# Kernel tuning notes

Hardware: AMD Instinct MI355X
Metric: run time of the kernel (lower is better)

Reference implementation:

```python
import jax, jax.numpy as jnp
import numpy as np

EPS = 1e-5
K_GROUP = 8  # k_group_size


def setup_inputs() -> dict:
    key = jax.random.key(0)
    ks = jax.random.split(key, 8)
    C = 384  # encoder_channel
    rn = lambda k, s: (jax.random.normal(k, s, dtype=jnp.float32) * 0.05)
    return {
        "point_groups": jax.random.normal(ks[0], (4, 256, 32, 3), dtype=jnp.float32),
        # first_conv: Conv1d(3,128,1)+BN+ReLU+Conv1d(128,256,1)
        "W1": rn(ks[1], (128, 3)), "b1": jnp.zeros(128, jnp.float32),
        "gamma1": jnp.ones(128, jnp.float32), "beta1": jnp.zeros(128, jnp.float32),
        "W2": rn(ks[2], (256, 128)), "b2": jnp.zeros(256, jnp.float32),
        # second_conv: Conv1d(512,512,1)+BN+ReLU+Conv1d(512,C,1)
        "W3": rn(ks[3], (512, 512)), "b3": jnp.zeros(512, jnp.float32),
        "gamma3": jnp.ones(512, jnp.float32), "beta3": jnp.zeros(512, jnp.float32),
        "W4": rn(ks[4], (C, 512)), "b4": jnp.zeros(C, jnp.float32),
        # K_Norm affine (out_dim = C, matching declared parameter shapes)
        "alpha": jnp.ones((1, 1, 1, C), jnp.float32),
        "beta_aff": jnp.zeros((1, 1, 1, C), jnp.float32),
        # fusion_layer: Conv1d(2C,C,1)+BN+ReLU
        "Wf": rn(ks[5], (C, 2 * C)), "bf": jnp.zeros(C, jnp.float32),
        "gammaf": jnp.ones(C, jnp.float32), "betaf": jnp.zeros(C, jnp.float32),
    }


def _conv1x1(x, W, b):  # x: (B,Cin,L), W: (Cout,Cin)
    return jnp.einsum("bcl,oc->bol", x, W) + b[None, :, None]


def _bn(x, gamma, beta):  # training-mode BatchNorm1d over (batch, length)
    mu = jnp.mean(x, axis=(0, 2), keepdims=True)
    var = jnp.var(x, axis=(0, 2), keepdims=True)
    xh = (x - mu) * jax.lax.rsqrt(var + EPS)
    return xh * gamma[None, :, None] + beta[None, :, None]


def reference(point_groups, W1, b1, gamma1, beta1, W2, b2, W3, b3, gamma3, beta3,
              W4, b4, alpha, beta_aff, Wf, bf, gammaf, betaf):
    bs, g, n, _ = point_groups.shape
    C = W4.shape[0]
    pg = point_groups.reshape(bs * g, n, 3)  # (B', n, 3)

    # first_conv stack
    f = _conv1x1(pg.transpose(0, 2, 1), W1, b1)           # (B',128,n)
    f = jax.nn.relu(_bn(f, gamma1, beta1))
    f = _conv1x1(f, W2, b2)                               # (B',256,n)
    fg = jnp.max(f, axis=2, keepdims=True)                # (B',256,1)
    f = jnp.concatenate([jnp.broadcast_to(fg, f.shape), f], axis=1)  # (B',512,n)

    # second_conv stack
    f = _conv1x1(f, W3, b3)
    f = jax.nn.relu(_bn(f, gamma3, beta3))
    f = _conv1x1(f, W4, b4)                               # (B',C,n)
    feat = f.transpose(0, 2, 1)                           # (B',n,C)

    # KNN within each group (self included, as in KNN(xyz,xyz))
    sq = jnp.sum(pg * pg, axis=-1)                        # (B',n)
    d = sq[:, :, None] + sq[:, None, :] - 2.0 * jnp.einsum("bnc,bmc->bnm", pg, pg)
    _, idx = jax.lax.top_k(-d, K_GROUP)                   # (B',n,K)

    gather = jax.vmap(lambda a, i: a[i])
    knn_x = gather(feat, idx)                             # (B',n,K,C)

    # K_Norm: center-relative normalization by global scalar std (torch.std, ddof=1)
    mean_x = feat[:, :, None, :]
    dx = knn_x - mean_x
    std_x = jnp.std(dx, ddof=1)
    knn_x = dx / (std_x + EPS)
    knn_x = alpha * knn_x + beta_aff                      # (B',n,K,C)

    enhanced = jnp.mean(knn_x, axis=2)                    # mean over K -> (B',n,C)
    enhanced = jnp.mean(enhanced, axis=1)                 # pool over n -> (B',C)

    fg2 = jnp.max(f, axis=2)                              # (B',C)
    fused_in = jnp.concatenate([fg2, enhanced], axis=1)[:, :, None]  # (B',2C,1)
    fused = jax.nn.relu(_bn(_conv1x1(fused_in, Wf, bf), gammaf, betaf))[:, :, 0]
    return fused.reshape(bs, g, C)
```

## Files before the change

kernel.cpp:

```cpp
#include <hip/hip_runtime.h>
#include <math.h>

#define EPS 1e-5f

typedef __attribute__((ext_vector_type(8))) short s16x8;
typedef __attribute__((ext_vector_type(4))) float f32x4;

__device__ __forceinline__ unsigned short f2bf(float x) {
    unsigned u = __float_as_uint(x);
    u += 0x7fffu + ((u >> 16) & 1u);
    return (unsigned short)(u >> 16);
}
__device__ __forceinline__ float bf2f(unsigned short h) {
    return __uint_as_float(((unsigned)h) << 16);
}
__device__ __forceinline__ unsigned long long pack4bf(float a, float b, float c, float d) {
    return (unsigned long long)f2bf(a)
         | ((unsigned long long)f2bf(b) << 16)
         | ((unsigned long long)f2bf(c) << 32)
         | ((unsigned long long)f2bf(d) << 48);
}

template<int CTRL>
__device__ __forceinline__ float dppmov(float x) {
    return __int_as_float(__builtin_amdgcn_update_dpp(
        0, __float_as_int(x), CTRL, 0xF, 0xF, true));
}
__device__ __forceinline__ float red16_sum(float x) {
    x += dppmov<0xB1>(x);
    x += dppmov<0x4E>(x);
    x += dppmov<0x141>(x);
    x += dppmov<0x140>(x);
    return x;
}
__device__ __forceinline__ float red16_max(float x) {
    x = fmaxf(x, dppmov<0xB1>(x));
    x = fmaxf(x, dppmov<0x4E>(x));
    x = fmaxf(x, dppmov<0x141>(x));
    x = fmaxf(x, dppmov<0x140>(x));
    return x;
}

__global__ __launch_bounds__(128) void k1_conv1_knn(
    const float* __restrict__ pg, const float* __restrict__ W1,
    const float* __restrict__ b1,
    const float* __restrict__ W2, const float* __restrict__ W3,
    const float* __restrict__ W4, const float* __restrict__ Wf,
    unsigned short* __restrict__ h1b, float* __restrict__ p1s, float* __restrict__ p1q,
    int* __restrict__ idxw,
    unsigned short* __restrict__ W2b, unsigned short* __restrict__ W3b,
    unsigned short* __restrict__ W4b, unsigned short* __restrict__ Wfb)
{
    __shared__ float pgs[96];
    __shared__ float sqs[32];
    if (blockIdx.x >= 1024) {
        const int i = (blockIdx.x - 1024) * 128 + threadIdx.x;
        if (i < 32768)  W2b[i] = f2bf(W2[i]);
        if (i < 262144) W3b[i] = f2bf(W3[i]);
        if (i < 196608) W4b[i] = f2bf(W4[i]);
        if (i < 294912) Wfb[i] = f2bf(Wf[i]);
        return;
    }
    const int b = blockIdx.x;
    const int t = threadIdx.x;
    if (t < 96) pgs[t] = pg[b * 96 + t];
    __syncthreads();
    if (t < 32) {
        float x = pgs[t*3+0], y = pgs[t*3+1], z = pgs[t*3+2];
        sqs[t] = x*x + y*y + z*z;
    }
    __syncthreads();
    {
        const float w0 = W1[t*3+0], w1 = W1[t*3+1], w2 = W1[t*3+2];
        const float bb = b1[t];
        float s = 0.f, q = 0.f;
        unsigned short* hcol = h1b + (size_t)b*4096 + t;
        #pragma unroll
        for (int l = 0; l < 32; ++l) {
            float v = fmaf(w2, pgs[l*3+2], fmaf(w1, pgs[l*3+1], fmaf(w0, pgs[l*3+0], bb)));
            hcol[l*128] = f2bf(v); s += v; q += v*v;
        }
        p1s[b*128 + t] = s;
        p1q[b*128 + t] = q;
    }
    if (t < 32) {
        const float xl = pgs[t*3+0], yl = pgs[t*3+1], zl = pgs[t*3+2];
        const float sql = sqs[t];
        float dist[32];
        #pragma unroll
        for (int m = 0; m < 32; ++m) {
            float dot = xl*pgs[m*3+0] + yl*pgs[m*3+1] + zl*pgs[m*3+2];
            dist[m] = sql + sqs[m] - 2.f*dot;
        }
        unsigned used = 0u;
        int* orow = idxw + b*256 + t*8;
        #pragma unroll
        for (int j = 0; j < 8; ++j) {
            float best = 3.4e38f; int bi = 0;
            #pragma unroll
            for (int m = 0; m < 32; ++m) {
                if (!((used >> m) & 1u) && dist[m] < best) { best = dist[m]; bi = m; }
            }
            used |= (1u << bi);
            orow[j] = bi;
        }
    }
}

__global__ __launch_bounds__(256) void k_bn_fin2(
    const float* __restrict__ ps, const float* __restrict__ pq,
    int nPart, int nChan, float invN,
    const float* __restrict__ gamma, const float* __restrict__ beta,
    float* __restrict__ scale, float* __restrict__ shift)
{
    const int ob = blockIdx.x * 4;
    const int t = threadIdx.x;
    const int co = t & 3, i0 = t >> 2;
    float s = 0.f, q = 0.f;
    for (int i = i0; i < nPart; i += 64) {
        s += ps[(size_t)i*nChan + ob + co];
        q += pq[(size_t)i*nChan + ob + co];
    }
    #pragma unroll
    for (int off = 32; off >= 4; off >>= 1) {
        s += __shfl_down(s, off, 64);
        q += __shfl_down(q, off, 64);
    }
    __shared__ float ss[4][4], qs[4][4];
    const int wid = t >> 6, lane = t & 63;
    if (lane < 4) { ss[wid][lane] = s; qs[wid][lane] = q; }
    __syncthreads();
    if (t < 4) {
        float S = ss[0][t] + ss[1][t] + ss[2][t] + ss[3][t];
        float Q = qs[0][t] + qs[1][t] + qs[2][t] + qs[3][t];
        const int o = ob + t;
        float mu  = S * invN;
        float var = Q * invN - mu*mu;
        float sc  = gamma[o] * rsqrtf(var + EPS);
        scale[o] = sc;
        shift[o] = beta[o] - mu * sc;
    }
}

__global__ __launch_bounds__(1024, 8) void k3_mfma(
    const unsigned short* __restrict__ h1b,
    const float* __restrict__ scale1, const float* __restrict__ shift1,
    const unsigned short* __restrict__ W2b, const float* __restrict__ b2,
    const unsigned short* __restrict__ W3b, const float* __restrict__ b3,
    unsigned short* __restrict__ h3b, float* __restrict__ p3s, float* __restrict__ p3q)
{
    const int g0 = blockIdx.x * 2;
    const int t = threadIdx.x;
    __shared__ __align__(16) unsigned short SB[26128];
    unsigned short* B1  = SB;
    unsigned short* F2  = SB + 8704;
    unsigned short* FGB = SB + 25600;

    {
        const int l = t >> 4, c0 = (t & 15) * 8;
        const int g = g0 + (l >> 5);
        s16x8 hv = *(const s16x8*)(h1b + (size_t)g*4096 + (l & 31)*128 + c0);
        unsigned short ov[8];
        #pragma unroll
        for (int e = 0; e < 8; ++e) {
            int c = c0 + e;
            float v = fmaxf(fmaf(bf2f((unsigned short)hv[e]), scale1[c], shift1[c]), 0.f);
            ov[e] = f2bf(v);
        }
        uint4 o4;
        o4.x = (unsigned)ov[0] | ((unsigned)ov[1] << 16);
        o4.y = (unsigned)ov[2] | ((unsigned)ov[3] << 16);
        o4.z = (unsigned)ov[4] | ((unsigned)ov[5] << 16);
        o4.w = (unsigned)ov[6] | ((unsigned)ov[7] << 16);
        *(uint4*)&B1[l*136 + c0] = o4;
    }
    __syncthreads();

    const int wave = t >> 6;
    const int lane = t & 63;
    const int m    = lane & 15;
    const int quad = lane >> 4;

    f32x4 acc2[4];
    #pragma unroll
    for (int n = 0; n < 4; ++n)
        acc2[n] = (f32x4){0.f, 0.f, 0.f, 0.f};

    #pragma unroll
    for (int kt = 0; kt < 4; ++kt) {
        s16x8 bv[4];
        #pragma unroll
        for (int nt = 0; nt < 4; ++nt)
            bv[nt] = *(const s16x8*)&B1[(nt*16 + m)*136 + kt*32 + quad*8];
        s16x8 av = *(const s16x8*)(W2b + (size_t)(wave*16 + m)*128 + kt*32 + quad*8);
        #pragma unroll
        for (int nt = 0; nt < 4; ++nt)
            acc2[nt] = __builtin_amdgcn_mfma_f32_16x16x32_bf16(av, bv[nt], acc2[nt], 0, 0, 0);
    }

    {
        const int o0 = wave*16 + quad*4;
        #pragma unroll
        for (int r = 0; r < 4; ++r) {
            float bb = b2[o0 + r];
            #pragma unroll
            for (int nt = 0; nt < 4; ++nt) acc2[nt][r] += bb;
        }
        #pragma unroll
        for (int nt = 0; nt < 4; ++nt) {
            const int row = nt*16 + m;
            *(unsigned long long*)&F2[row*264 + o0] =
                pack4bf(acc2[nt][0], acc2[nt][1], acc2[nt][2], acc2[nt][3]);
        }
        float f0[4], f1[4];
        #pragma unroll
        for (int r = 0; r < 4; ++r) {
            f0[r] = red16_max(fmaxf(acc2[0][r], acc2[1][r]));
            f1[r] = red16_max(fmaxf(acc2[2][r], acc2[3][r]));
        }
        if (m == 0) {
            *(unsigned long long*)&FGB[o0]       = pack4bf(f0[0], f0[1], f0[2], f0[3]);
            *(unsigned long long*)&FGB[264 + o0] = pack4bf(f1[0], f1[1], f1[2], f1[3]);
        }
    }
    __syncthreads();

    unsigned short* dst = h3b + (size_t)blockIdx.x * 32768;
    #pragma unroll
    for (int mt = 0; mt < 2; ++mt) {
        const int ot = wave*2 + mt;
        const int o0 = ot*16 + quad*4;

        f32x4 facc = (f32x4){0.f, 0.f, 0.f, 0.f};
        #pragma unroll
        for (int kt = 0; kt < 8; ++kt) {
            s16x8 bg = *(const s16x8*)&FGB[(m & 1)*264 + kt*32 + quad*8];
            s16x8 av = *(const s16x8*)(W3b + (size_t)(ot*16 + m)*512 + kt*32 + quad*8);
            facc = __builtin_amdgcn_mfma_f32_16x16x32_bf16(av, bg, facc, 0, 0, 0);
        }

        f32x4 acc3[4];
        #pragma unroll
        for (int r = 0; r < 4; ++r) {
            float self = facc[r];
            float oth  = dppmov<0xB1>(self);
            float fg_g0 = (m & 1) ? oth : self;
            float fg_g1 = (m & 1) ? self : oth;
            float bb = b3[o0 + r];
            acc3[0][r] = bb + fg_g0;
            acc3[1][r] = bb + fg_g0;
            acc3[2][r] = bb + fg_g1;
            acc3[3][r] = bb + fg_g1;
        }

        #pragma unroll
        for (int kt = 0; kt < 8; ++kt) {
            s16x8 bv[4];
            #pragma unroll
            for (int nt = 0; nt < 4; ++nt)
                bv[nt] = *(const s16x8*)&F2[(nt*16 + m)*264 + kt*32 + quad*8];
            s16x8 av = *(const s16x8*)(W3b + (size_t)(ot*16 + m)*512 + 256 + kt*32 + quad*8);
            #pragma unroll
            for (int nt = 0; nt < 4; ++nt)
                acc3[nt] = __builtin_amdgcn_mfma_f32_16x16x32_bf16(av, bv[nt], acc3[nt], 0, 0, 0);
        }

        float s[4], q[4];
        #pragma unroll
        for (int r = 0; r < 4; ++r) {
            float x0 = acc3[0][r], x1 = acc3[1][r];
            float x2 = acc3[2][r], x3 = acc3[3][r];
            s[r] = (x0 + x1) + (x2 + x3);
            q[r] = (x0*x0 + x1*x1) + (x2*x2 + x3*x3);
        }
        {
            unsigned long long u0 = pack4bf(acc3[0][0], acc3[0][1], acc3[0][2], acc3[0][3]);
            unsigned long long u1 = pack4bf(acc3[1][0], acc3[1][1], acc3[1][2], acc3[1][3]);
            unsigned long long u2 = pack4bf(acc3[2][0], acc3[2][1], acc3[2][2], acc3[2][3]);
            unsigned long long u3 = pack4bf(acc3[3][0], acc3[3][1], acc3[3][2], acc3[3][3]);
            unsigned short* p = dst + (size_t)(ot*64 + lane) * 16;
            *(uint4*)(p)     = make_uint4((unsigned)u0, (unsigned)(u0 >> 32), (unsigned)u1, (unsigned)(u1 >> 32));
            *(uint4*)(p + 8) = make_uint4((unsigned)u2, (unsigned)(u2 >> 32), (unsigned)u3, (unsigned)(u3 >> 32));
        }
        #pragma unroll
        for (int r = 0; r < 4; ++r) {
            s[r] = red16_sum(s[r]);
            q[r] = red16_sum(q[r]);
        }
        if (m == 0) {
            #pragma unroll
            for (int r = 0; r < 4; ++r) {
                p3s[(size_t)blockIdx.x*512 + o0 + r] = s[r];
                p3q[(size_t)blockIdx.x*512 + o0 + r] = q[r];
            }
        }
    }
}

__global__ __launch_bounds__(512, 4) void k5_mfma(
    const unsigned short* __restrict__ h3b,
    const float* __restrict__ scale3, const float* __restrict__ shift3,
    const unsigned short* __restrict__ W4b, const float* __restrict__ b4,
    const int* __restrict__ idxw,
    float* __restrict__ fg2, float* __restrict__ A,
    float* __restrict__ S1p, float* __restrict__ S2p)
{
    const int g0 = blockIdx.x * 2;
    const int t = threadIdx.x;
    __shared__ __align__(16) unsigned short SB[33280];
    unsigned short* B4 = SB;
    unsigned short* XT = SB;
    unsigned short* Mm = SB + 30720;
    __shared__ int icnt[2][32];
    __shared__ float r1[2][8], r2[2][8];

    {
        const uint4* src = (const uint4*)(h3b + (size_t)blockIdx.x * 32768);
        for (int i = t; i < 4096; i += 512) {
            uint4 hv = src[i];
            const int flat16 = i >> 1, half = i & 1;
            const int ln = flat16 & 63, m2 = ln & 15, q2 = ln >> 4;
            const int wm = flat16 >> 6;
            const int o0 = wm*16 + q2*4;
            const float4 sc = *(const float4*)(scale3 + o0);
            const float4 sh = *(const float4*)(shift3 + o0);
            const int rowa = (half*2)*16 + m2;
            float a0 = fmaxf(fmaf(bf2f((unsigned short)(hv.x       )), sc.x, sh.x), 0.f);
            float a1 = fmaxf(fmaf(bf2f((unsigned short)(hv.x >> 16 )), sc.y, sh.y), 0.f);
            float a2 = fmaxf(fmaf(bf2f((unsigned short)(hv.y       )), sc.z, sh.z), 0.f);
            float a3 = fmaxf(fmaf(bf2f((unsigned short)(hv.y >> 16 )), sc.w, sh.w), 0.f);
            float b0 = fmaxf(fmaf(bf2f((unsigned short)(hv.z       )), sc.x, sh.x), 0.f);
            float b1 = fmaxf(fmaf(bf2f((unsigned short)(hv.z >> 16 )), sc.y, sh.y), 0.f);
            float b2 = fmaxf(fmaf(bf2f((unsigned short)(hv.w       )), sc.z, sh.z), 0.f);
            float b3 = fmaxf(fmaf(bf2f((unsigned short)(hv.w >> 16 )), sc.w, sh.w), 0.f);
            *(unsigned long long*)&B4[rowa*520 + o0]        = pack4bf(a0, a1, a2, a3);
            *(unsigned long long*)&B4[(rowa + 16)*520 + o0] = pack4bf(b0, b1, b2, b3);
        }
    }
    if (t < 64) icnt[t >> 5][t & 31] = 0;
    __syncthreads();

    const int wave = t >> 6;
    const int lane = t & 63;
    const int m    = lane & 15;
    const int quad = lane >> 4;

    f32x4 acc4[3][4];
    #pragma unroll
    for (int mt = 0; mt < 3; ++mt)
        #pragma unroll
        for (int n = 0; n < 4; ++n)
            acc4[mt][n] = (f32x4){0.f, 0.f, 0.f, 0.f};

    #pragma unroll 4
    for (int kt = 0; kt < 16; ++kt) {
        s16x8 bv[4];
        #pragma unroll
        for (int nt = 0; nt < 4; ++nt)
            bv[nt] = *(const s16x8*)&B4[(nt*16 + m)*520 + kt*32 + quad*8];
        #pragma unroll
        for (int mt = 0; mt < 3; ++mt) {
            s16x8 av = *(const s16x8*)(W4b + (size_t)(wave*48 + mt*16 + m)*512 + kt*32 + quad*8);
            #pragma unroll
            for (int nt = 0; nt < 4; ++nt)
                acc4[mt][nt] = __builtin_amdgcn_mfma_f32_16x16x32_bf16(av, bv[nt], acc4[mt][nt], 0, 0, 0);
        }
    }

    #pragma unroll
    for (int mt = 0; mt < 3; ++mt) {
        const int o0 = wave*48 + mt*16 + quad*4;
        float f0[4], f1[4];
        #pragma unroll
        for (int r = 0; r < 4; ++r) {
            float bb = b4[o0 + r];
            #pragma unroll
            for (int nt = 0; nt < 4; ++nt) acc4[mt][nt][r] += bb;
            f0[r] = red16_max(fmaxf(acc4[mt][0][r], acc4[mt][1][r]));
            f1[r] = red16_max(fmaxf(acc4[mt][2][r], acc4[mt][3][r]));
        }
        if (m == 0) {
            #pragma unroll
            for (int r = 0; r < 4; ++r) {
                fg2[(size_t)g0*384 + o0 + r]     = f0[r];
                fg2[(size_t)(g0+1)*384 + o0 + r] = f1[r];
            }
        }
    }
    __syncthreads();

    #pragma unroll
    for (int mt = 0; mt < 3; ++mt) {
        const int o0 = wave*48 + mt*16 + quad*4;
        #pragma unroll
        for (int nt = 0; nt < 4; ++nt) {
            const int g = nt >> 1;
            const int l = (nt & 1)*16 + m;
            unsigned short* xg = XT + g*15360;
            #pragma unroll
            for (int r = 0; r < 4; ++r)
                xg[(o0 + r)*40 + l] = f2bf(acc4[mt][nt][r]);
        }
    }
    if (t < 64) {
        const int g = t >> 5, l = t & 31;
        uint4 z = make_uint4(0u, 0u, 0u, 0u);
        #pragma unroll
        for (int i = 0; i < 5; ++i)
            *(uint4*)&Mm[g*1280 + l*40 + i*8] = z;
    }
    __syncthreads();

    if (t < 64) {
        const int g = t >> 5, l = t & 31;
        const int* ip = idxw + (size_t)(g0 + g)*256 + l*8;
        #pragma unroll
        for (int j = 0; j < 8; ++j) {
            int ix = ip[j];
            Mm[g*1280 + l*40 + ix] = 0x3F80;
            atomicAdd(&icnt[g][ix], 1);
        }
    }
    __syncthreads();

    float s1loc[2] = {0.f, 0.f}, s2loc[2] = {0.f, 0.f};
    #pragma unroll
    for (int g = 0; g < 2; ++g) {
        const float c0 = (float)icnt[g][m];
        const float c1 = (float)icnt[g][m + 16];
        const float w0 = c0 - 8.f, u0 = c0 + 8.f;
        const float w1 = c1 - 8.f, u1 = c1 + 8.f;
        #pragma unroll
        for (int mt = 0; mt < 3; ++mt) {
            const int o0 = wave*48 + mt*16 + quad*4;
            float Ap[4];
            #pragma unroll
            for (int r = 0; r < 4; ++r) {
                const float x0 = acc4[mt][g*2 + 0][r];
                const float x1 = acc4[mt][g*2 + 1][r];
                Ap[r] = w0*x0 + w1*x1;
                s1loc[g] += Ap[r];
                s2loc[g] += u0*x0*x0 + u1*x1*x1;
            }
            #pragma unroll
            for (int r = 0; r < 4; ++r)
                Ap[r] = red16_sum(Ap[r]);
            if (m == 0) {
                #pragma unroll
                for (int r = 0; r < 4; ++r)
                    A[(size_t)(g0 + g)*384 + o0 + r] = Ap[r];
            }
        }
    }

    #pragma unroll
    for (int g = 0; g < 2; ++g) {
        const unsigned short* xg = XT + g*15360;
        float cross = 0.f;
        #pragma unroll
        for (int lt = 0; lt < 2; ++lt) {
            s16x8 af = *(const s16x8*)&Mm[g*1280 + (lt*16 + m)*40 + quad*8];
            #pragma unroll
            for (int i = 0; i < 3; ++i) {
                const int oc = (wave*3 + i)*16 + m;
                s16x8 bfv = *(const s16x8*)&xg[oc*40 + quad*8];
                f32x4 sa = __builtin_amdgcn_mfma_f32_16x16x32_bf16(
                    af, bfv, (f32x4){0.f, 0.f, 0.f, 0.f}, 0, 0, 0);
                #pragma unroll
                for (int r = 0; r < 4; ++r) {
                    const int lp = lt*16 + quad*4 + r;
                    cross = fmaf(bf2f(xg[oc*40 + lp]), sa[r], cross);
                }
            }
        }
        s2loc[g] -= 2.f * cross;
    }

    #pragma unroll
    for (int g = 0; g < 2; ++g) {
        float sA = s1loc[g], sQ = s2loc[g];
        #pragma unroll
        for (int off = 32; off > 0; off >>= 1) {
            sA += __shfl_down(sA, off, 64);
            sQ += __shfl_down(sQ, off, 64);
        }
        if (lane == 0) { r1[g][wave] = sA; r2[g][wave] = sQ; }
    }
    __syncthreads();
    if (t < 2) {
        float S = 0.f, Q = 0.f;
        #pragma unroll
        for (int w = 0; w < 8; ++w) { S += r1[t][w]; Q += r2[t][w]; }
        S1p[g0 + t] = S;
        S2p[g0 + t] = Q;
    }
}

__global__ __launch_bounds__(384) void k7_fused(
    const float* __restrict__ fg2, const float* __restrict__ A,
    const float* __restrict__ alpha, const float* __restrict__ beta_aff,
    const float* __restrict__ S1p, const float* __restrict__ S2p,
    const unsigned short* __restrict__ Wfb, const float* __restrict__ bf,
    float* __restrict__ hf, float* __restrict__ pfs, float* __restrict__ pfq)
{
    const int blk    = blockIdx.x;
    const int slice  = blk >> 2;
    const int msplit = blk & 3;
    const int g0     = slice * 16;
    const int obase  = msplit * 96;
    const int t = threadIdx.x;
    __shared__ __align__(16) char smem[24832];
    unsigned short* xfb = (unsigned short*)smem;
    float* OTf = (float*)smem;
    __shared__ double rs[6], rq[6];
    __shared__ float stdsh;

    {
        double s = 0.0, q = 0.0;
        for (int i = t; i < 1024; i += 384) { s += (double)S1p[i]; q += (double)S2p[i]; }
        #pragma unroll
        for (int off = 32; off > 0; off >>= 1) {
            s += __shfl_down(s, off, 64);
            q += __shfl_down(q, off, 64);
        }
        if ((t & 63) == 0) { rs[t >> 6] = s; rq[t >> 6] = q; }
        __syncthreads();
        if (t == 0) {
            double S = 0.0, Q = 0.0;
            #pragma unroll
            for (int w = 0; w < 6; ++w) { S += rs[w]; Q += rq[w]; }
            const double N = 1024.0 * 32.0 * 8.0 * 384.0;
            double var = (Q - S*S/N) / (N - 1.0);
            stdsh = (float)sqrt(var);
        }
        __syncthreads();
    }
    const float inv = 1.f / (256.f * (stdsh + EPS));

    for (int i = t; i < 16*96; i += 384) {
        const int row = i / 96, c8 = (i % 96) * 8;
        const int g = g0 + row;
        float e[8];
        if (c8 < 384) {
            const float4* s0 = (const float4*)(fg2 + (size_t)g*384 + c8);
            float4 v0 = s0[0], v1 = s0[1];
            e[0]=v0.x; e[1]=v0.y; e[2]=v0.z; e[3]=v0.w;
            e[4]=v1.x; e[5]=v1.y; e[6]=v1.z; e[7]=v1.w;
        } else {
            const int cc = c8 - 384;
            const float4* s0 = (const float4*)(A + (size_t)g*384 + cc);
            float4 v0 = s0[0], v1 = s0[1];
            float av[8] = {v0.x,v0.y,v0.z,v0.w,v1.x,v1.y,v1.z,v1.w};
            #pragma unroll
            for (int j = 0; j < 8; ++j)
                e[j] = fmaf(alpha[cc+j] * inv, av[j], beta_aff[cc+j]);
        }
        uint4 o4;
        o4.x = (unsigned)f2bf(e[0]) | ((unsigned)f2bf(e[1]) << 16);
        o4.y = (unsigned)f2bf(e[2]) | ((unsigned)f2bf(e[3]) << 16);
        o4.z = (unsigned)f2bf(e[4]) | ((unsigned)f2bf(e[5]) << 16);
        o4.w = (unsigned)f2bf(e[6]) | ((unsigned)f2bf(e[7]) << 16);
        *(uint4*)&xfb[row*776 + c8] = o4;
    }
    __syncthreads();

    const int wave = t >> 6;
    const int lane = t & 63;
    const int m    = lane & 15;
    const int quad = lane >> 4;

    f32x4 acc = (f32x4){0.f, 0.f, 0.f, 0.f};
    #pragma unroll 4
    for (int kt = 0; kt < 24; ++kt) {
        s16x8 bv = *(const s16x8*)&xfb[m*776 + kt*32 + quad*8];
        s16x8 av = *(const s16x8*)(Wfb + (size_t)(obase + wave*16 + m)*768 + kt*32 + quad*8);
        acc = __builtin_amdgcn_mfma_f32_16x16x32_bf16(av, bv, acc, 0, 0, 0);
    }

    {
        const int o0 = obase + wave*16 + quad*4;
        float s[4], q[4];
        #pragma unroll
        for (int r = 0; r < 4; ++r) {
            acc[r] += bf[o0 + r];
            s[r] = red16_sum(acc[r]);
            q[r] = red16_sum(acc[r]*acc[r]);
        }
        if (m == 0) {
            #pragma unroll
            for (int r = 0; r < 4; ++r) {
                pfs[(size_t)slice*384 + o0 + r] = s[r];
                pfq[(size_t)slice*384 + o0 + r] = q[r];
            }
        }
    }
    __syncthreads();

    {
        const int lo0 = wave*16 + quad*4;
        #pragma unroll
        for (int r = 0; r < 4; ++r)
            OTf[m*100 + lo0 + r] = acc[r];
    }
    __syncthreads();

    {
        const int grp = t / 24, c4 = t % 24;
        float4 v = *(const float4*)&OTf[grp*100 + c4*4];
        *(float4*)(hf + (size_t)(g0 + grp)*384 + obase + c4*4) = v;
    }
}

__global__ __launch_bounds__(384) void k9_out(
    const float* __restrict__ hf,
    const float* __restrict__ pfs, const float* __restrict__ pfq,
    const float* __restrict__ gammaf, const float* __restrict__ betaf,
    float* __restrict__ out)
{
    const int blk = blockIdx.x, t = threadIdx.x;
    float S = 0.f, Q = 0.f;
    #pragma unroll 8
    for (int i = 0; i < 64; ++i) {
        S += pfs[(size_t)i*384 + t];
        Q += pfq[(size_t)i*384 + t];
    }
    const float mu  = S * (1.f/1024.f);
    const float var = Q * (1.f/1024.f) - mu*mu;
    const float sc  = gammaf[t] * rsqrtf(var + EPS);
    const float sh  = betaf[t] - mu * sc;
    const size_t base = (size_t)blk * 8 * 384;
    #pragma unroll
    for (int g = 0; g < 8; ++g) {
        float v = fmaf(hf[base + g*384 + t], sc, sh);
        out[base + g*384 + t] = fmaxf(v, 0.f);
    }
}

extern "C" void kernel_launch(void* const* d_in, const int* in_sizes, int n_in,
                              void* d_out, int out_size, void* d_ws, size_t ws_size,
                              hipStream_t stream) {
    const float* pg      = (const float*)d_in[0];
    const float* W1      = (const float*)d_in[1];
    const float* b1      = (const float*)d_in[2];
    const float* gamma1  = (const float*)d_in[3];
    const float* beta1   = (const float*)d_in[4];
    const float* W2      = (const float*)d_in[5];
    const float* b2      = (const float*)d_in[6];
    const float* W3      = (const float*)d_in[7];
    const float* b3      = (const float*)d_in[8];
    const float* gamma3  = (const float*)d_in[9];
    const float* beta3   = (const float*)d_in[10];
    const float* W4      = (const float*)d_in[11];
    const float* b4      = (const float*)d_in[12];
    const float* alpha   = (const float*)d_in[13];
    const float* beta_af = (const float*)d_in[14];
    const float* Wf      = (const float*)d_in[15];
    const float* bf      = (const float*)d_in[16];
    const float* gammaf  = (const float*)d_in[17];
    const float* betaf   = (const float*)d_in[18];
    float* out = (float*)d_out;

    float* w = (float*)d_ws;
    unsigned short* h1b = (unsigned short*)w; w += 1024*4096/2;
    unsigned short* h3b = (unsigned short*)w; w += 1024*16384/2;
    unsigned short* W2b = (unsigned short*)w; w += 32768/2;
    unsigned short* W3b = (unsigned short*)w; w += 262144/2;
    unsigned short* W4b = (unsigned short*)w; w += 196608/2;
    unsigned short* Wfb = (unsigned short*)w; w += 294912/2;
    float* hf     = w;  w += 1024*384;
    float* fg2    = w;  w += 1024*384;
    float* A      = w;  w += 1024*384;
    float* p1s    = w;  w += 1024*128;
    float* p1q    = w;  w += 1024*128;
    float* p3s    = w;  w += 1024*512;
    float* p3q    = w;  w += 1024*512;
    float* pfs    = w;  w += 64*384;
    float* pfq    = w;  w += 64*384;
    float* S1p    = w;  w += 1024;
    float* S2p    = w;  w += 1024;
    float* scale1 = w;  w += 128;
    float* shift1 = w;  w += 128;
    float* scale3 = w;  w += 512;
    float* shift3 = w;  w += 512;
    int*   idxw   = (int*)w;  w += 1024*256;

    hipLaunchKernelGGL(k1_conv1_knn, dim3(1024 + 2304), dim3(128), 0, stream,
                       pg, W1, b1, W2, W3, W4, Wf,
                       h1b, p1s, p1q, idxw, W2b, W3b, W4b, Wfb);
    hipLaunchKernelGGL(k_bn_fin2, dim3(32), dim3(256), 0, stream,
                       p1s, p1q, 1024, 128, 1.f/32768.f, gamma1, beta1, scale1, shift1);
    hipLaunchKernelGGL(k3_mfma, dim3(512), dim3(1024), 0, stream,
                       h1b, scale1, shift1, W2b, b2, W3b, b3, h3b, p3s, p3q);
    hipLaunchKernelGGL(k_bn_fin2, dim3(128), dim3(256), 0, stream,
                       p3s, p3q, 512, 512, 1.f/32768.f, gamma3, beta3, scale3, shift3);
    hipLaunchKernelGGL(k5_mfma, dim3(512), dim3(512), 0, stream,
                       h3b, scale3, shift3, W4b, b4, idxw, fg2, A, S1p, S2p);
    hipLaunchKernelGGL(k7_fused, dim3(256), dim3(384), 0, stream,
                       fg2, A, alpha, beta_af, S1p, S2p, Wfb, bf, hf, pfs, pfq);
    hipLaunchKernelGGL(k9_out, dim3(128), dim3(384), 0, stream,
                       hf, pfs, pfq, gammaf, betaf, out);
}
```

Before: 204.8 us.

## Replace BN finalize kernels with binned atomic partial sums folded into consumers

The per-block BatchNorm partial sums are now accumulated with float atomics into 8 bins per channel instead of being written to large partial arrays. The two standalone finalize kernels are removed, and each consumer kernel recomputes scale and shift from the bins into shared memory. This drops two kernel launches and their serialization gaps. In exchange, it adds a memset, atomic contention on the bins, and redundant finalize work in every consumer block, and atomic ordering makes the float sums nondeterministic.

```diff
diff --git a/kernel.cpp b/kernel.cpp
--- a/kernel.cpp
+++ b/kernel.cpp
@@ -46,7 +46,8 @@
     const float* __restrict__ b1,
     const float* __restrict__ W2, const float* __restrict__ W3,
     const float* __restrict__ W4, const float* __restrict__ Wf,
-    unsigned short* __restrict__ h1b, float* __restrict__ p1s, float* __restrict__ p1q,
+    unsigned short* __restrict__ h1b,
+    float* __restrict__ p1sb, float* __restrict__ p1qb,
     int* __restrict__ idxw,
     unsigned short* __restrict__ W2b, unsigned short* __restrict__ W3b,
     unsigned short* __restrict__ W4b, unsigned short* __restrict__ Wfb)
@@ -80,8 +81,8 @@
             float v = fmaf(w2, pgs[l*3+2], fmaf(w1, pgs[l*3+1], fmaf(w0, pgs[l*3+0], bb)));
             hcol[l*128] = f2bf(v); s += v; q += v*v;
         }
-        p1s[b*128 + t] = s;
-        p1q[b*128 + t] = q;
+        atomicAdd(&p1sb[((b & 7) << 7) + t], s);
+        atomicAdd(&p1qb[((b & 7) << 7) + t], q);
     }
     if (t < 32) {
         const float xl = pgs[t*3+0], yl = pgs[t*3+1], zl = pgs[t*3+2];
@@ -107,47 +108,14 @@
     }
 }
 
-__global__ __launch_bounds__(256) void k_bn_fin2(
-    const float* __restrict__ ps, const float* __restrict__ pq,
-    int nPart, int nChan, float invN,
-    const float* __restrict__ gamma, const float* __restrict__ beta,
-    float* __restrict__ scale, float* __restrict__ shift)
-{
-    const int ob = blockIdx.x * 4;
-    const int t = threadIdx.x;
-    const int co = t & 3, i0 = t >> 2;
-    float s = 0.f, q = 0.f;
-    for (int i = i0; i < nPart; i += 64) {
-        s += ps[(size_t)i*nChan + ob + co];
-        q += pq[(size_t)i*nChan + ob + co];
-    }
-    #pragma unroll
-    for (int off = 32; off >= 4; off >>= 1) {
-        s += __shfl_down(s, off, 64);
-        q += __shfl_down(q, off, 64);
-    }
-    __shared__ float ss[4][4], qs[4][4];
-    const int wid = t >> 6, lane = t & 63;
-    if (lane < 4) { ss[wid][lane] = s; qs[wid][lane] = q; }
-    __syncthreads();
-    if (t < 4) {
-        float S = ss[0][t] + ss[1][t] + ss[2][t] + ss[3][t];
-        float Q = qs[0][t] + qs[1][t] + qs[2][t] + qs[3][t];
-        const int o = ob + t;
-        float mu  = S * invN;
-        float var = Q * invN - mu*mu;
-        float sc  = gamma[o] * rsqrtf(var + EPS);
-        scale[o] = sc;
-        shift[o] = beta[o] - mu * sc;
-    }
-}
-
 __global__ __launch_bounds__(1024, 8) void k3_mfma(
     const unsigned short* __restrict__ h1b,
-    const float* __restrict__ scale1, const float* __restrict__ shift1,
+    const float* __restrict__ gamma1, const float* __restrict__ beta1,
+    const float* __restrict__ p1sb, const float* __restrict__ p1qb,
     const unsigned short* __restrict__ W2b, const float* __restrict__ b2,
     const unsigned short* __restrict__ W3b, const float* __restrict__ b3,
-    unsigned short* __restrict__ h3b, float* __restrict__ p3s, float* __restrict__ p3q)
+    unsigned short* __restrict__ h3b,
+    float* __restrict__ p3sb, float* __restrict__ p3qb)
 {
     const int g0 = blockIdx.x * 2;
     const int t = threadIdx.x;
@@ -155,6 +123,22 @@
     unsigned short* B1  = SB;
     unsigned short* F2  = SB + 8704;
     unsigned short* FGB = SB + 25600;
+    __shared__ __align__(16) float sc1s[128], sh1s[128];
+
+    if (t < 128) {
+        float S = 0.f, Q = 0.f;
+        #pragma unroll
+        for (int bb = 0; bb < 8; ++bb) {
+            S += p1sb[(bb << 7) + t];
+            Q += p1qb[(bb << 7) + t];
+        }
+        float mu  = S * (1.f/32768.f);
+        float var = Q * (1.f/32768.f) - mu*mu;
+        float sc  = gamma1[t] * rsqrtf(var + EPS);
+        sc1s[t] = sc;
+        sh1s[t] = beta1[t] - mu * sc;
+    }
+    __syncthreads();
 
     {
         const int l = t >> 4, c0 = (t & 15) * 8;
@@ -164,7 +148,7 @@
         #pragma unroll
         for (int e = 0; e < 8; ++e) {
             int c = c0 + e;
-            float v = fmaxf(fmaf(bf2f((unsigned short)hv[e]), scale1[c], shift1[c]), 0.f);
+            float v = fmaxf(fmaf(bf2f((unsigned short)hv[e]), sc1s[c], sh1s[c]), 0.f);
             ov[e] = f2bf(v);
         }
         uint4 o4;
@@ -226,6 +210,7 @@
     __syncthreads();
 
     unsigned short* dst = h3b + (size_t)blockIdx.x * 32768;
+    const int binbase = (blockIdx.x & 7) << 9;
     #pragma unroll
     for (int mt = 0; mt < 2; ++mt) {
         const int ot = wave*2 + mt;
@@ -290,8 +275,8 @@
         if (m == 0) {
             #pragma unroll
             for (int r = 0; r < 4; ++r) {
-                p3s[(size_t)blockIdx.x*512 + o0 + r] = s[r];
-                p3q[(size_t)blockIdx.x*512 + o0 + r] = q[r];
+                atomicAdd(&p3sb[binbase + o0 + r], s[r]);
+                atomicAdd(&p3qb[binbase + o0 + r], q[r]);
             }
         }
     }
@@ -299,7 +284,8 @@
 
 __global__ __launch_bounds__(512, 4) void k5_mfma(
     const unsigned short* __restrict__ h3b,
-    const float* __restrict__ scale3, const float* __restrict__ shift3,
+    const float* __restrict__ gamma3, const float* __restrict__ beta3,
+    const float* __restrict__ p3sb, const float* __restrict__ p3qb,
     const unsigned short* __restrict__ W4b, const float* __restrict__ b4,
     const int* __restrict__ idxw,
     float* __restrict__ fg2, float* __restrict__ A,
@@ -311,8 +297,25 @@
     unsigned short* B4 = SB;
     unsigned short* XT = SB;
     unsigned short* Mm = SB + 30720;
+    __shared__ __align__(16) float sc3s[512], sh3s[512];
     __shared__ int icnt[2][32];
     __shared__ float r1[2][8], r2[2][8];
+
+    {
+        float S = 0.f, Q = 0.f;
+        #pragma unroll
+        for (int bb = 0; bb < 8; ++bb) {
+            S += p3sb[(bb << 9) + t];
+            Q += p3qb[(bb << 9) + t];
+        }
+        float mu  = S * (1.f/32768.f);
+        float var = Q * (1.f/32768.f) - mu*mu;
+        float sc  = gamma3[t] * rsqrtf(var + EPS);
+        sc3s[t] = sc;
+        sh3s[t] = beta3[t] - mu * sc;
+    }
+    if (t < 64) icnt[t >> 5][t & 31] = 0;
+    __syncthreads();
 
     {
         const uint4* src = (const uint4*)(h3b + (size_t)blockIdx.x * 32768);
@@ -322,8 +325,8 @@
             const int ln = flat16 & 63, m2 = ln & 15, q2 = ln >> 4;
             const int wm = flat16 >> 6;
             const int o0 = wm*16 + q2*4;
-            const float4 sc = *(const float4*)(scale3 + o0);
-            const float4 sh = *(const float4*)(shift3 + o0);
+            const float4 sc = *(const float4*)&sc3s[o0];
+            const float4 sh = *(const float4*)&sh3s[o0];
             const int rowa = (half*2)*16 + m2;
             float a0 = fmaxf(fmaf(bf2f((unsigned short)(hv.x       )), sc.x, sh.x), 0.f);
             float a1 = fmaxf(fmaf(bf2f((unsigned short)(hv.x >> 16 )), sc.y, sh.y), 0.f);
@@ -337,7 +340,6 @@
             *(unsigned long long*)&B4[(rowa + 16)*520 + o0] = pack4bf(b0, b1, b2, b3);
         }
     }
-    if (t < 64) icnt[t >> 5][t & 31] = 0;
     __syncthreads();
 
     const int wave = t >> 6;
@@ -670,31 +672,26 @@
     float* hf     = w;  w += 1024*384;
     float* fg2    = w;  w += 1024*384;
     float* A      = w;  w += 1024*384;
-    float* p1s    = w;  w += 1024*128;
-    float* p1q    = w;  w += 1024*128;
-    float* p3s    = w;  w += 1024*512;
-    float* p3q    = w;  w += 1024*512;
+    float* p1sb   = w;  w += 8*128;
+    float* p1qb   = w;  w += 8*128;
+    float* p3sb   = w;  w += 8*512;
+    float* p3qb   = w;  w += 8*512;
     float* pfs    = w;  w += 64*384;
     float* pfq    = w;  w += 64*384;
     float* S1p    = w;  w += 1024;
     float* S2p    = w;  w += 1024;
-    float* scale1 = w;  w += 128;
-    float* shift1 = w;  w += 128;
-    float* scale3 = w;  w += 512;
-    float* shift3 = w;  w += 512;
     int*   idxw   = (int*)w;  w += 1024*256;
 
+    hipMemsetAsync(p1sb, 0, (8*128*2 + 8*512*2) * sizeof(float), stream);
     hipLaunchKernelGGL(k1_conv1_knn, dim3(1024 + 2304), dim3(128), 0, stream,
                        pg, W1, b1, W2, W3, W4, Wf,
-                       h1b, p1s, p1q, idxw, W2b, W3b, W4b, Wfb);
-    hipLaunchKernelGGL(k_bn_fin2, dim3(32), dim3(256), 0, stream,
-                       p1s, p1q, 1024, 128, 1.f/32768.f, gamma1, beta1, scale1, shift1);
+                       h1b, p1sb, p1qb, idxw, W2b, W3b, W4b, Wfb);
     hipLaunchKernelGGL(k3_mfma, dim3(512), dim3(1024), 0, stream,
-                       h1b, scale1, shift1, W2b, b2, W3b, b3, h3b, p3s, p3q);
-    hipLaunchKernelGGL(k_bn_fin2, dim3(128), dim3(256), 0, stream,
-                       p3s, p3q, 512, 512, 1.f/32768.f, gamma3, beta3, scale3, shift3);
+                       h1b, gamma1, beta1, p1sb, p1qb, W2b, b2, W3b, b3,
+                       h3b, p3sb, p3qb);
     hipLaunchKernelGGL(k5_mfma, dim3(512), dim3(512), 0, stream,
-                       h3b, scale3, shift3, W4b, b4, idxw, fg2, A, S1p, S2p);
+                       h3b, gamma3, beta3, p3sb, p3qb, W4b, b4, idxw,
+                       fg2, A, S1p, S2p);
     hipLaunchKernelGGL(k7_fused, dim3(256), dim3(384), 0, stream,
                        fg2, A, alpha, beta_af, S1p, S2p, Wfb, bf, hf, pfs, pfq);
     hipLaunchKernelGGL(k9_out, dim3(128), dim3(384), 0, stream,
```

Result: faster. 195.5 us (-4.5%).
